# Performance work log

Hardware: AMD Instinct MI355X
Metric: run time of the kernel (lower is better)

The kernel has to match this reference:

```python
import jax, jax.numpy as jnp
import numpy as np

B, S, H = 4, 1024, 2048
NQ, NKV, D = 32, 4, 128
EPS = 1e-6
THETA = 1e6


def setup_inputs() -> dict:
    key = jax.random.key(0)
    k1, k2, k3 = jax.random.split(key, 3)
    hidden = jax.random.normal(k1, (B, S, H), jnp.float32) * 0.02
    w_qkv = jax.random.normal(k2, (H, (NQ + 2 * NKV) * D), jnp.float32) * 0.02
    w_o = jax.random.normal(k3, (NQ * D, H), jnp.float32) * 0.02
    q_norm_w = jnp.ones((D,), jnp.float32)
    k_norm_w = jnp.ones((D,), jnp.float32)
    # rotary tables, broadcast to [B, S, D]
    inv_freq = 1.0 / (THETA ** (jnp.arange(0, D, 2, dtype=jnp.float32) / D))
    freqs = jnp.arange(S, dtype=jnp.float32)[:, None] * inv_freq[None, :]  # [S, D/2]
    emb = jnp.concatenate([freqs, freqs], axis=-1)  # [S, D]
    cos = jnp.broadcast_to(jnp.cos(emb)[None], (B, S, D))
    sin = jnp.broadcast_to(jnp.sin(emb)[None], (B, S, D))
    return {"hidden": hidden, "w_qkv": w_qkv, "w_o": w_o,
            "q_norm_w": q_norm_w, "k_norm_w": k_norm_w, "cos": cos, "sin": sin}


def _rms_norm(x, w):
    xf = x.astype(jnp.float32)
    var = jnp.mean(xf * xf, axis=-1, keepdims=True)
    return (w * (xf * jax.lax.rsqrt(var + EPS))).astype(x.dtype)


def _rotate_half(x):
    h = x.shape[-1] // 2
    return jnp.concatenate([-x[..., h:], x[..., :h]], axis=-1)


def reference(hidden, w_qkv, w_o, q_norm_w, k_norm_w, cos, sin):
    b, s, _ = hidden.shape
    qkv = jnp.einsum('bsh,he->bse', hidden, w_qkv)
    q = qkv[..., : NQ * D].reshape(b, s, NQ, D)
    k = qkv[..., NQ * D: (NQ + NKV) * D].reshape(b, s, NKV, D)
    v = qkv[..., (NQ + NKV) * D:].reshape(b, s, NKV, D)

    # per-head RMSNorm on Q and K
    q = _rms_norm(q, q_norm_w)
    k = _rms_norm(k, k_norm_w)

    # fused RoPE (rotate-half), cos/sin broadcast over heads
    c = cos[:, :, None, :]
    sn = sin[:, :, None, :]
    q = q * c + _rotate_half(q) * sn
    k = k * c + _rotate_half(k) * sn

    # GQA causal flash-attention (prefill, sparse_mode=3 -> causal)
    g = NQ // NKV
    qg = q.reshape(b, s, NKV, g, D)
    scale = 1.0 / jnp.sqrt(jnp.asarray(D, hidden.dtype))
    scores = jnp.einsum('bqkgd,bskd->bkgqs', qg, k) * scale  # [B,NKV,g,S,S]
    causal = jnp.tril(jnp.ones((s, s), bool))
    scores = jnp.where(causal[None, None, None], scores, jnp.finfo(scores.dtype).min)
    probs = jax.nn.softmax(scores, axis=-1)
    out = jnp.einsum('bkgqs,bskd->bqkgd', probs, v).reshape(b, s, NQ * D)
    return jnp.einsum('bse,eh->bsh', out, w_o)
```

## Files before the change

kernel.cpp:

```cpp
#include <hip/hip_runtime.h>

#define BB 4
#define SS 1024
#define HH 2048
#define NQH 32
#define NKVH 4
#define DD 128
#define EQKV 5120

typedef __attribute__((ext_vector_type(8))) short s8v;
typedef __attribute__((ext_vector_type(4))) short s4v;
typedef __attribute__((ext_vector_type(4))) float f4v;

__device__ __forceinline__ unsigned short f2bf(float f) {
  unsigned int u = __builtin_bit_cast(unsigned int, f);
  u += 0x7fffu + ((u >> 16) & 1u);
  return (unsigned short)(u >> 16);
}
__device__ __forceinline__ float bf2f(unsigned short s) {
  unsigned int u = ((unsigned int)s) << 16;
  return __builtin_bit_cast(float, u);
}

__device__ __forceinline__ void async16(unsigned short* lds, const unsigned short* g) {
  __builtin_amdgcn_global_load_lds(
      (const __attribute__((address_space(1))) unsigned int*)g,
      (__attribute__((address_space(3))) unsigned int*)lds, 16, 0, 0);
}


__global__ __launch_bounds__(256) void cvt_bf16(const float* __restrict__ in,
                                                unsigned short* __restrict__ out, int n) {
  int i = (blockIdx.x * 256 + threadIdx.x) * 4;
  if (i >= n) return;
  f4v v = *reinterpret_cast<const f4v*>(in + i);
  s4v o;
#pragma unroll
  for (int j = 0; j < 4; ++j) o[j] = (short)f2bf(v[j]);
  *reinterpret_cast<s4v*>(out + i) = o;
}

__global__ __launch_bounds__(256) void transpose_cvt(const float* __restrict__ in,
                                                     unsigned short* __restrict__ out,
                                                     int K, int N) {
  __shared__ unsigned short T[64][65];
  const int k0 = blockIdx.y * 64, n0 = blockIdx.x * 64;
  const int t = threadIdx.x;
  const int r = t >> 4, c4 = (t & 15) * 4;
#pragma unroll
  for (int i = 0; i < 4; ++i) {
    f4v v = *reinterpret_cast<const f4v*>(&in[(size_t)(k0 + r + i * 16) * N + n0 + c4]);
#pragma unroll
    for (int j = 0; j < 4; ++j) T[r + i * 16][c4 + j] = f2bf(v[j]);
  }
  __syncthreads();
#pragma unroll
  for (int i = 0; i < 4; ++i) {
    int n = r + i * 16;
    s4v o;
#pragma unroll
    for (int j = 0; j < 4; ++j) o[j] = (short)T[c4 + j][n];
    *reinterpret_cast<s4v*>(&out[(size_t)(n0 + n) * K + k0 + c4]) = o;
  }
}

__global__ __launch_bounds__(256) void vtrans(const unsigned short* __restrict__ qkv,
                                              unsigned short* __restrict__ Vt) {
  __shared__ unsigned short T[64][68];
  const int s0 = blockIdx.x * 64;
  const int d0 = blockIdx.y * 64;
  const int bk = blockIdx.z;
  const int b = bk >> 2, hkv = bk & 3;
  const int t = threadIdx.x;
  const int r = t >> 4, c4 = (t & 15) * 4;
  const unsigned short* src = qkv + (size_t)(b * SS + s0) * EQKV + (NQH + NKVH + hkv) * DD + d0;
#pragma unroll
  for (int i = 0; i < 4; ++i) {
    int s = r + i * 16;
    s4v v = *reinterpret_cast<const s4v*>(src + (size_t)s * EQKV + c4);
    *reinterpret_cast<s4v*>(&T[s][c4]) = v;
  }
  __syncthreads();
#pragma unroll
  for (int i = 0; i < 4; ++i) {
    int d = r + i * 16;
    s4v o;
#pragma unroll
    for (int j = 0; j < 4; ++j) o[j] = (short)T[c4 + j][d];
    *reinterpret_cast<s4v*>(&Vt[((size_t)bk * DD + d0 + d) * SS + s0 + c4]) = o;
  }
}

template <bool CF32>
__global__ __launch_bounds__(256) void gemm_128(const unsigned short* __restrict__ A,
                                                const unsigned short* __restrict__ Bt,
                                                void* __restrict__ Cp,
                                                int M, int N, int K, int lda) {
  __shared__ unsigned short BUF[2][16384];
  const int tid = threadIdx.x;
  const int ln = tid & 63, w = tid >> 6;
  const int la = ln & 15, quad = ln >> 4;
  const int wm = (w >> 1) * 64, wn = (w & 1) * 64;

  const int G = gridDim.x, cpx = G >> 3;
  const int swz = (blockIdx.x & 7) * cpx + (blockIdx.x >> 3);
  const int ytiles = M >> 7;
  const int by = swz % ytiles, bx = swz / ytiles;
  const int m0 = by * 128, n0 = bx * 128;

  f4v acc[4][4] = {};

  const int srow = w * 32 + (ln >> 3);
  const int sch = ((ln & 7) ^ ((ln >> 3) & 7)) * 8;
  const unsigned short* pA = A + (size_t)(m0 + srow) * lda + sch;
  const unsigned short* pB = Bt + (size_t)(n0 + srow) * K + sch;

#define STAGE(bf, koff)                                                        \
  _Pragma("unroll") for (int j = 0; j < 4; ++j) {                              \
    async16(&BUF[bf][(w * 4 + j) * 512], pA + (size_t)(j * 8) * lda + (koff)); \
    async16(&BUF[bf][8192 + (w * 4 + j) * 512], pB + (size_t)(j * 8) * K + (koff)); \
  }

  STAGE(0, 0)
  __syncthreads();

  const int NT = K >> 6;
  int cur = 0;
  for (int t = 0; t < NT; ++t) {
    const int kn = (t + 1 < NT) ? (t + 1) * 64 : t * 64;
    STAGE(cur ^ 1, kn)
    s8v a[4][2], b[4][2];
#pragma unroll
    for (int f = 0; f < 4; ++f)
#pragma unroll
      for (int kh = 0; kh < 2; ++kh) {
        const int slot = ((kh * 4 + quad) ^ (la & 7)) * 8;
        a[f][kh] = *reinterpret_cast<const s8v*>(&BUF[cur][(wm + f * 16 + la) * 64 + slot]);
        b[f][kh] = *reinterpret_cast<const s8v*>(&BUF[cur][8192 + (wn + f * 16 + la) * 64 + slot]);
      }
    __builtin_amdgcn_s_setprio(1);
#pragma unroll
    for (int kh = 0; kh < 2; ++kh)
#pragma unroll
      for (int mf = 0; mf < 4; ++mf)
#pragma unroll
        for (int nf = 0; nf < 4; ++nf)
          acc[mf][nf] = __builtin_amdgcn_mfma_f32_16x16x32_bf16(a[mf][kh], b[nf][kh], acc[mf][nf], 0, 0, 0);
    __builtin_amdgcn_s_setprio(0);
    __syncthreads();
    cur ^= 1;
  }
#undef STAGE

#pragma unroll
  for (int mf = 0; mf < 4; ++mf)
#pragma unroll
    for (int nf = 0; nf < 4; ++nf)
#pragma unroll
      for (int r = 0; r < 4; ++r) {
        int row = m0 + wm + mf * 16 + quad * 4 + r;
        int col = n0 + wn + nf * 16 + la;
        if constexpr (CF32) ((float*)Cp)[(size_t)row * N + col] = acc[mf][nf][r];
        else ((unsigned short*)Cp)[(size_t)row * N + col] = f2bf(acc[mf][nf][r]);
      }
}

__global__ __launch_bounds__(512) void attn2(unsigned short* __restrict__ qkv,
                                             const unsigned short* __restrict__ Vt) {
  const int idx = blockIdx.x;
  const int tile = 7 - (idx >> 7);
  const int h = idx & 31;
  const int b = (idx >> 5) & 3;
  const int hkv = h >> 3;
  const int tid = threadIdx.x;
  const int ln = tid & 63, w = tid >> 6;
  const int la = ln & 15, quad = ln >> 4;
  const int qr0 = tile * 128;
  __shared__ unsigned short Ks[64 * 128];
  __shared__ unsigned short Vts[128 * 64];
  __shared__ unsigned short Ps[8][16][64];

  const size_t rowb = (size_t)b * SS;
  const int wq0 = qr0 + w * 16;
  const int wqb = wq0 & ~63;
  s8v qf[4];
  {
    const unsigned short* qrow = qkv + (rowb + wq0 + la) * EQKV + h * DD;
#pragma unroll
    for (int t = 0; t < 4; ++t) qf[t] = *reinterpret_cast<const s8v*>(qrow + t * 32 + quad * 8);
  }
  const unsigned short* kcol = qkv + (NQH + hkv) * DD;
  const unsigned short* vtb = Vt + (size_t)(b * NKVH + hkv) * DD * SS;

  float m_[4], ls[4];
  f4v acc[8] = {};
#pragma unroll
  for (int r = 0; r < 4; ++r) { m_[r] = -1.0e30f; ls[r] = 0.f; }

  const float SC = 0.08838834764831845f;
  const int nkb = 2 * tile + 2;
  for (int kb = 0; kb < nkb; ++kb) {
    const int key0 = kb * 64;
    __syncthreads();
#pragma unroll
    for (int i = 0; i < 2; ++i) {
      int row = w * 8 + i * 4 + (ln >> 4);
      int chunk = (ln & 15) ^ (row & 15);
      async16(&Ks[(w * 8 + i * 4) * 128],
              kcol + (rowb + key0 + row) * EQKV + chunk * 8);
    }
#pragma unroll
    for (int i = 0; i < 2; ++i) {
      int row = w * 16 + i * 8 + (ln >> 3);
      int chunk = (ln & 7) ^ (ln >> 3);
      async16(&Vts[(w * 16 + i * 8) * 64],
              vtb + (size_t)row * SS + key0 + chunk * 8);
    }
    __syncthreads();
    if (key0 > wqb) continue;
    f4v sc[4];
#pragma unroll
    for (int kt = 0; kt < 4; ++kt) {
      f4v z = {};
#pragma unroll
      for (int t = 0; t < 4; ++t) {
        s8v kf = *reinterpret_cast<const s8v*>(&Ks[(kt * 16 + la) * 128 + ((t * 4 + quad) ^ la) * 8]);
        z = __builtin_amdgcn_mfma_f32_16x16x32_bf16(qf[t], kf, z, 0, 0, 0);
      }
      sc[kt] = z;
    }
    const bool diag = (key0 == wqb);
    float pmax[4];
#pragma unroll
    for (int r = 0; r < 4; ++r) {
      if (diag) {
        int q = wq0 + quad * 4 + r;
#pragma unroll
        for (int kt = 0; kt < 4; ++kt)
          if (key0 + kt * 16 + la > q) sc[kt][r] = -1.0e30f;
      }
      pmax[r] = fmaxf(fmaxf(sc[0][r], sc[1][r]), fmaxf(sc[2][r], sc[3][r]));
    }
    int need = 0;
#pragma unroll
    for (int r = 0; r < 4; ++r) need |= (pmax[r] > m_[r] + 64.0f) ? 1 : 0;
    if (__any(need)) {
#pragma unroll
      for (int r = 0; r < 4; ++r) {
        float mx = pmax[r];
#pragma unroll
        for (int off = 8; off >= 1; off >>= 1) mx = fmaxf(mx, __shfl_xor(mx, off));
        float mnew = fmaxf(m_[r], mx);
        float al = __expf((m_[r] - mnew) * SC);
        m_[r] = mnew;
        ls[r] *= al;
#pragma unroll
        for (int nt = 0; nt < 8; ++nt) acc[nt][r] *= al;
      }
    }
#pragma unroll
    for (int r = 0; r < 4; ++r) {
      const int row = quad * 4 + r;
      const float mS = m_[r] * SC;
#pragma unroll
      for (int kt = 0; kt < 4; ++kt) {
        float p = __expf(__builtin_fmaf(sc[kt][r], SC, -mS));
        ls[r] += p;
        int col = kt * 16 + la;
        Ps[w][row][(((col >> 3) ^ (row & 7)) << 3) | (col & 7)] = f2bf(p);
      }
    }
#pragma unroll
    for (int c = 0; c < 2; ++c) {
      s8v pf = *reinterpret_cast<const s8v*>(&Ps[w][la][(((c * 4 + quad) ^ (la & 7)) << 3)]);
#pragma unroll
      for (int nt = 0; nt < 8; ++nt) {
        s8v vf = *reinterpret_cast<const s8v*>(
            &Vts[(nt * 16 + la) * 64 + ((c * 4 + quad) ^ (la & 7)) * 8]);
        acc[nt] = __builtin_amdgcn_mfma_f32_16x16x32_bf16(pf, vf, acc[nt], 0, 0, 0);
      }
    }
  }
#pragma unroll
  for (int r = 0; r < 4; ++r)
#pragma unroll
    for (int off = 8; off >= 1; off >>= 1) ls[r] += __shfl_xor(ls[r], off);
#pragma unroll
  for (int nt = 0; nt < 8; ++nt)
#pragma unroll
    for (int r = 0; r < 4; ++r) {
      int q = wq0 + quad * 4 + r;
      qkv[(rowb + q) * EQKV + h * DD + nt * 16 + la] = f2bf(acc[nt][r] / ls[r]);
    }
}

template <bool AF32, bool BF32, bool CF32>
__global__ __launch_bounds__(256) void gemm_t(const void* __restrict__ Ap,
                                              const void* __restrict__ Bp,
                                              void* __restrict__ Cp,
                                              int M, int N, int K, int lda) {
  __shared__ unsigned short As[64][40];
  __shared__ unsigned short Bs[64][40];
  const int tid  = threadIdx.x;
  const int lane = tid & 63;
  const int wave = tid >> 6;
  const int la   = lane & 15;
  const int quad = lane >> 4;
  const int m0 = blockIdx.y * 64;
  const int n0 = blockIdx.x * 64;
  const int wm = (wave >> 1) * 32;
  const int wn = (wave & 1) * 32;
  f4v acc[2][2] = {};
  const int ar = tid >> 2, ac = (tid & 3) * 8;
  const int bk = tid >> 3, bn = (tid & 7) * 8;
  for (int k0 = 0; k0 < K; k0 += 32) {
    s8v av;
    if constexpr (AF32) {
      const float* a = (const float*)Ap + (size_t)(m0 + ar) * lda + ac + k0;
      f4v v0 = *reinterpret_cast<const f4v*>(a);
      f4v v1 = *reinterpret_cast<const f4v*>(a + 4);
#pragma unroll
      for (int j = 0; j < 4; ++j) { av[j] = (short)f2bf(v0[j]); av[j + 4] = (short)f2bf(v1[j]); }
    } else {
      av = *reinterpret_cast<const s8v*>((const unsigned short*)Ap + (size_t)(m0 + ar) * lda + ac + k0);
    }
    unsigned short bvs[8];
    if constexpr (BF32) {
      const float* bp = (const float*)Bp + (size_t)(k0 + bk) * N + n0 + bn;
      f4v v0 = *reinterpret_cast<const f4v*>(bp);
      f4v v1 = *reinterpret_cast<const f4v*>(bp + 4);
#pragma unroll
      for (int j = 0; j < 4; ++j) { bvs[j] = f2bf(v0[j]); bvs[j + 4] = f2bf(v1[j]); }
    } else {
      s8v bv = *reinterpret_cast<const s8v*>((const unsigned short*)Bp + (size_t)(k0 + bk) * N + n0 + bn);
#pragma unroll
      for (int j = 0; j < 8; ++j) bvs[j] = (unsigned short)bv[j];
    }
    *reinterpret_cast<s8v*>(&As[ar][ac]) = av;
#pragma unroll
    for (int j = 0; j < 8; ++j) Bs[bn + j][bk] = bvs[j];
    __syncthreads();
#pragma unroll
    for (int mi = 0; mi < 2; ++mi) {
      s8v af = *reinterpret_cast<const s8v*>(&As[wm + mi * 16 + la][quad * 8]);
#pragma unroll
      for (int ni = 0; ni < 2; ++ni) {
        s8v bfr = *reinterpret_cast<const s8v*>(&Bs[wn + ni * 16 + la][quad * 8]);
        acc[mi][ni] = __builtin_amdgcn_mfma_f32_16x16x32_bf16(af, bfr, acc[mi][ni], 0, 0, 0);
      }
    }
    __syncthreads();
  }
#pragma unroll
  for (int mi = 0; mi < 2; ++mi)
#pragma unroll
    for (int ni = 0; ni < 2; ++ni)
#pragma unroll
      for (int r = 0; r < 4; ++r) {
        int row = m0 + wm + mi * 16 + quad * 4 + r;
        int col = n0 + wn + ni * 16 + la;
        if constexpr (CF32) ((float*)Cp)[(size_t)row * N + col] = acc[mi][ni][r];
        else ((unsigned short*)Cp)[(size_t)row * N + col] = f2bf(acc[mi][ni][r]);
      }
}

__global__ __launch_bounds__(64) void attn_slow(unsigned short* __restrict__ qkv) {
  const int tile = blockIdx.x;
  const int h = blockIdx.y;
  const int b = blockIdx.z;
  const int hkv = h >> 3;
  const int lane = threadIdx.x;
  const int la = lane & 15;
  const int quad = lane >> 4;
  const int qr0 = tile * 16;
  __shared__ unsigned short P[16][32];
  __shared__ unsigned short V[32][128];
  const size_t base = (size_t)b * SS * EQKV;
  s8v qf[4];
  {
    const unsigned short* qrow = qkv + base + (size_t)(qr0 + la) * EQKV + h * DD;
#pragma unroll
    for (int t = 0; t < 4; ++t)
      qf[t] = *reinterpret_cast<const s8v*>(qrow + t * 32 + quad * 8);
  }
  const unsigned short* kbase = qkv + base + (NQH + hkv) * DD;
  const unsigned short* vbase = qkv + base + (NQH + NKVH + hkv) * DD;
  float m[4], l[4], al[4];
  f4v acc[8] = {};
#pragma unroll
  for (int r = 0; r < 4; ++r) { m[r] = -1.0e30f; l[r] = 0.f; }
  const float scale = 0.08838834764831845f;
  const int nkb = (qr0 + 16 + 31) >> 5;
  for (int kb = 0; kb < nkb; ++kb) {
    const int key0 = kb * 32;
    __syncthreads();
#pragma unroll
    for (int i = 0; i < 8; ++i) {
      int c = i * 64 + lane;
      int row = c >> 4, col = (c & 15) * 8;
      *reinterpret_cast<s8v*>(&V[row][col]) =
          *reinterpret_cast<const s8v*>(vbase + (size_t)(key0 + row) * EQKV + col);
    }
    f4v s0 = {}, s1 = {};
#pragma unroll
    for (int t = 0; t < 4; ++t) {
      s8v k0f = *reinterpret_cast<const s8v*>(kbase + (size_t)(key0 + la) * EQKV + t * 32 + quad * 8);
      s8v k1f = *reinterpret_cast<const s8v*>(kbase + (size_t)(key0 + 16 + la) * EQKV + t * 32 + quad * 8);
      s0 = __builtin_amdgcn_mfma_f32_16x16x32_bf16(qf[t], k0f, s0, 0, 0, 0);
      s1 = __builtin_amdgcn_mfma_f32_16x16x32_bf16(qf[t], k1f, s1, 0, 0, 0);
    }
#pragma unroll
    for (int r = 0; r < 4; ++r) {
      int q = qr0 + quad * 4 + r;
      float v0 = (key0 + la <= q) ? s0[r] * scale : -1.0e30f;
      float v1 = (key0 + 16 + la <= q) ? s1[r] * scale : -1.0e30f;
      float mx = fmaxf(v0, v1);
#pragma unroll
      for (int off = 8; off >= 1; off >>= 1) mx = fmaxf(mx, __shfl_xor(mx, off));
      float mnew = fmaxf(m[r], mx);
      float p0 = __expf(v0 - mnew);
      float p1 = __expf(v1 - mnew);
      al[r] = __expf(m[r] - mnew);
      m[r] = mnew;
      float rsum = p0 + p1;
#pragma unroll
      for (int off = 8; off >= 1; off >>= 1) rsum += __shfl_xor(rsum, off);
      l[r] = l[r] * al[r] + rsum;
      P[quad * 4 + r][la] = f2bf(p0);
      P[quad * 4 + r][la + 16] = f2bf(p1);
    }
#pragma unroll
    for (int nt = 0; nt < 8; ++nt)
#pragma unroll
      for (int r = 0; r < 4; ++r) acc[nt][r] *= al[r];
    __syncthreads();
    s8v pf = *reinterpret_cast<const s8v*>(&P[la][quad * 8]);
#pragma unroll
    for (int nt = 0; nt < 8; ++nt) {
      s8v vf;
#pragma unroll
      for (int j = 0; j < 8; ++j)
        vf[j] = (short)V[quad * 8 + j][nt * 16 + la];
      acc[nt] = __builtin_amdgcn_mfma_f32_16x16x32_bf16(pf, vf, acc[nt], 0, 0, 0);
    }
  }
#pragma unroll
  for (int nt = 0; nt < 8; ++nt)
#pragma unroll
    for (int r = 0; r < 4; ++r) {
      int q = qr0 + quad * 4 + r;
      qkv[base + (size_t)q * EQKV + h * DD + nt * 16 + la] = f2bf(acc[nt][r] / l[r]);
    }
}

__global__ __launch_bounds__(256) void norm_rope(unsigned short* __restrict__ qkv,
                                                 const float* __restrict__ qw,
                                                 const float* __restrict__ kw,
                                                 const float* __restrict__ cosp,
                                                 const float* __restrict__ sinp) {
  const int h = blockIdx.x;
  const int bs = blockIdx.y * 4 + (threadIdx.x >> 6);
  const int s = bs & (SS - 1);
  const int lane = threadIdx.x & 63;
  const int d0 = lane * 2;
  unsigned short* p = qkv + (size_t)bs * EQKV + h * DD + d0;
  unsigned int u = *reinterpret_cast<const unsigned int*>(p);
  float x0 = bf2f((unsigned short)(u & 0xffff));
  float x1 = bf2f((unsigned short)(u >> 16));
  float ss = x0 * x0 + x1 * x1;
#pragma unroll
  for (int off = 32; off >= 1; off >>= 1) ss += __shfl_xor(ss, off);
  float rs = rsqrtf(ss * (1.0f / 128.0f) + 1e-6f);
  const float* w = (h < NQH) ? qw : kw;
  float n0 = x0 * rs * w[d0];
  float n1 = x1 * rs * w[d0 + 1];
  float o0 = __shfl_xor(n0, 32);
  float o1 = __shfl_xor(n1, 32);
  float r0 = (lane < 32) ? -o0 : o0;
  float r1 = (lane < 32) ? -o1 : o1;
  float c0 = cosp[(size_t)s * DD + d0], c1 = cosp[(size_t)s * DD + d0 + 1];
  float s0 = sinp[(size_t)s * DD + d0], s1 = sinp[(size_t)s * DD + d0 + 1];
  float y0 = n0 * c0 + r0 * s0;
  float y1 = n1 * c1 + r1 * s1;
  unsigned int outv = (unsigned int)f2bf(y0) | ((unsigned int)f2bf(y1) << 16);
  *reinterpret_cast<unsigned int*>(p) = outv;
}

extern "C" void kernel_launch(void* const* d_in, const int* in_sizes, int n_in,
                              void* d_out, int out_size, void* d_ws, size_t ws_size,
                              hipStream_t stream) {
  const float* hidden = (const float*)d_in[0];
  const float* w_qkv  = (const float*)d_in[1];
  const float* w_o    = (const float*)d_in[2];
  const float* q_w    = (const float*)d_in[3];
  const float* k_w    = (const float*)d_in[4];
  const float* cosp   = (const float*)d_in[5];
  const float* sinp   = (const float*)d_in[6];
  float* out = (float*)d_out;

  const int M = BB * SS;
  const size_t szHid  = (size_t)M * HH;
  const size_t szWqkv = (size_t)HH * EQKV;
  const size_t szWo   = (size_t)(NQH * DD) * HH;
  const size_t szQkv  = (size_t)M * EQKV;
  const size_t need = (szHid + szWqkv + szWo + szQkv) * sizeof(unsigned short);

  if (ws_size >= need) {
    unsigned short* hb16  = (unsigned short*)d_ws;
    unsigned short* wqkvT = hb16 + szHid;
    unsigned short* woT   = wqkvT + szWqkv;
    unsigned short* qkv   = woT + szWo;
    unsigned short* Vt    = hb16;

    cvt_bf16<<<(int)(szHid / 1024), 256, 0, stream>>>(hidden, hb16, (int)szHid);
    transpose_cvt<<<dim3(EQKV / 64, HH / 64), 256, 0, stream>>>(w_qkv, wqkvT, HH, EQKV);
    transpose_cvt<<<dim3(HH / 64, (NQH * DD) / 64), 256, 0, stream>>>(w_o, woT, NQH * DD, HH);

    gemm_128<false><<<(M / 128) * (EQKV / 128), 256, 0, stream>>>(
        hb16, wqkvT, qkv, M, EQKV, HH, HH);
    vtrans<<<dim3(SS / 64, DD / 64, BB * NKVH), 256, 0, stream>>>(qkv, Vt);
    norm_rope<<<dim3(NQH + NKVH, M / 4), 256, 0, stream>>>(qkv, q_w, k_w, cosp, sinp);
    attn2<<<1024, 512, 0, stream>>>(qkv, Vt);
    gemm_128<true><<<(M / 128) * (HH / 128), 256, 0, stream>>>(
        qkv, woT, out, M, HH, NQH * DD, EQKV);
  } else {
    unsigned short* qkvb = (unsigned short*)d_ws;
    for (int b = 0; b < BB; ++b) {
      const float* hb = hidden + (size_t)b * SS * HH;
      float* ob = out + (size_t)b * SS * HH;
      gemm_t<true, true, false><<<dim3(EQKV / 64, SS / 64), 256, 0, stream>>>(
          hb, w_qkv, qkvb, SS, EQKV, HH, HH);
      norm_rope<<<dim3(NQH + NKVH, SS / 4), 256, 0, stream>>>(qkvb, q_w, k_w, cosp, sinp);
      attn_slow<<<dim3(SS / 16, NQH, 1), 64, 0, stream>>>(qkvb);
      gemm_t<false, true, true><<<dim3(HH / 64, SS / 64), 256, 0, stream>>>(
          qkvb, w_o, ob, SS, HH, NQH * DD, EQKV);
    }
  }
}
```

Baseline: 424.4 us.

## Fuse hidden fp32-to-bf16 conversion into QKV GEMM and Q norm/RoPE into attention

Removes the separate hidden-state bf16 conversion kernel. The QKV GEMM now loads fp32 A tiles into registers, converts them to bf16 and writes them to LDS after the MFMA block, overlapping the global loads with compute. Q-head RMSNorm and RoPE move into the attention kernel's Q fragment load, so norm_rope only processes the 4 K heads. This saves one full pass over hidden and the Q region of qkv. The cost is twice the A-operand global traffic inside the GEMM, more register pressure, and a synchronous load path in place of async LDS copies for A.

```diff
diff --git a/kernel.cpp b/kernel.cpp
--- a/kernel.cpp
+++ b/kernel.cpp
@@ -28,17 +28,6 @@
       (__attribute__((address_space(3))) unsigned int*)lds, 16, 0, 0);
 }
 
-
-__global__ __launch_bounds__(256) void cvt_bf16(const float* __restrict__ in,
-                                                unsigned short* __restrict__ out, int n) {
-  int i = (blockIdx.x * 256 + threadIdx.x) * 4;
-  if (i >= n) return;
-  f4v v = *reinterpret_cast<const f4v*>(in + i);
-  s4v o;
-#pragma unroll
-  for (int j = 0; j < 4; ++j) o[j] = (short)f2bf(v[j]);
-  *reinterpret_cast<s4v*>(out + i) = o;
-}
 
 __global__ __launch_bounds__(256) void transpose_cvt(const float* __restrict__ in,
                                                      unsigned short* __restrict__ out,
@@ -91,8 +80,8 @@
   }
 }
 
-template <bool CF32>
-__global__ __launch_bounds__(256) void gemm_128(const unsigned short* __restrict__ A,
+template <bool AF32, bool CF32>
+__global__ __launch_bounds__(256) void gemm_128(const void* __restrict__ Ap,
                                                 const unsigned short* __restrict__ Bt,
                                                 void* __restrict__ Cp,
                                                 int M, int N, int K, int lda) {
@@ -112,23 +101,58 @@
 
   const int srow = w * 32 + (ln >> 3);
   const int sch = ((ln & 7) ^ ((ln >> 3) & 7)) * 8;
-  const unsigned short* pA = A + (size_t)(m0 + srow) * lda + sch;
+  const unsigned short* pAh =
+      AF32 ? nullptr : (const unsigned short*)Ap + (size_t)(m0 + srow) * lda + sch;
+  const float* pAf =
+      AF32 ? (const float*)Ap + (size_t)(m0 + srow) * lda + (ln & 7) * 8 : nullptr;
   const unsigned short* pB = Bt + (size_t)(n0 + srow) * K + sch;
-
-#define STAGE(bf, koff)                                                        \
-  _Pragma("unroll") for (int j = 0; j < 4; ++j) {                              \
-    async16(&BUF[bf][(w * 4 + j) * 512], pA + (size_t)(j * 8) * lda + (koff)); \
-    async16(&BUF[bf][8192 + (w * 4 + j) * 512], pB + (size_t)(j * 8) * K + (koff)); \
-  }
-
-  STAGE(0, 0)
+  const int awr = srow * 64 + sch;
+
+#define STAGE_B(bf, koff)                                                           \
+  _Pragma("unroll") for (int j = 0; j < 4; ++j)                                     \
+    async16(&BUF[bf][8192 + (w * 4 + j) * 512], pB + (size_t)(j * 8) * K + (koff));
+#define STAGE_AH(bf, koff)                                                          \
+  _Pragma("unroll") for (int j = 0; j < 4; ++j)                                     \
+    async16(&BUF[bf][(w * 4 + j) * 512], pAh + (size_t)(j * 8) * lda + (koff));
+#define LOAD_AF(koff)                                                               \
+  _Pragma("unroll") for (int j = 0; j < 4; ++j) {                                   \
+    const float* p = pAf + (size_t)(j * 8) * lda + (koff);                          \
+    va[j][0] = *reinterpret_cast<const f4v*>(p);                                    \
+    va[j][1] = *reinterpret_cast<const f4v*>(p + 4);                                \
+  }
+#define WRITE_AF(bf)                                                                \
+  _Pragma("unroll") for (int j = 0; j < 4; ++j) {                                   \
+    s8v o;                                                                          \
+    _Pragma("unroll") for (int c = 0; c < 4; ++c) o[c] = (short)f2bf(va[j][0][c]);  \
+    _Pragma("unroll") for (int c = 0; c < 4; ++c) o[c + 4] = (short)f2bf(va[j][1][c]); \
+    *reinterpret_cast<s8v*>(&BUF[bf][awr + j * 512]) = o;                           \
+  }
+
+  {
+    f4v va[4][2];
+    if constexpr (AF32) {
+      LOAD_AF(0)
+      STAGE_B(0, 0)
+      WRITE_AF(0)
+    } else {
+      STAGE_AH(0, 0)
+      STAGE_B(0, 0)
+    }
+  }
   __syncthreads();
 
   const int NT = K >> 6;
   int cur = 0;
   for (int t = 0; t < NT; ++t) {
     const int kn = (t + 1 < NT) ? (t + 1) * 64 : t * 64;
-    STAGE(cur ^ 1, kn)
+    f4v va[4][2];
+    if constexpr (AF32) {
+      LOAD_AF(kn)
+      STAGE_B(cur ^ 1, kn)
+    } else {
+      STAGE_AH(cur ^ 1, kn)
+      STAGE_B(cur ^ 1, kn)
+    }
     s8v a[4][2], b[4][2];
 #pragma unroll
     for (int f = 0; f < 4; ++f)
@@ -147,10 +171,14 @@
         for (int nf = 0; nf < 4; ++nf)
           acc[mf][nf] = __builtin_amdgcn_mfma_f32_16x16x32_bf16(a[mf][kh], b[nf][kh], acc[mf][nf], 0, 0, 0);
     __builtin_amdgcn_s_setprio(0);
+    if constexpr (AF32) { WRITE_AF(cur ^ 1) }
     __syncthreads();
     cur ^= 1;
   }
-#undef STAGE
+#undef STAGE_B
+#undef STAGE_AH
+#undef LOAD_AF
+#undef WRITE_AF
 
 #pragma unroll
   for (int mf = 0; mf < 4; ++mf)
@@ -166,7 +194,10 @@
 }
 
 __global__ __launch_bounds__(512) void attn2(unsigned short* __restrict__ qkv,
-                                             const unsigned short* __restrict__ Vt) {
+                                             const unsigned short* __restrict__ Vt,
+                                             const float* __restrict__ qnw,
+                                             const float* __restrict__ cosp,
+                                             const float* __restrict__ sinp) {
   const int idx = blockIdx.x;
   const int tile = 7 - (idx >> 7);
   const int h = idx & 31;
@@ -186,8 +217,46 @@
   s8v qf[4];
   {
     const unsigned short* qrow = qkv + (rowb + wq0 + la) * EQKV + h * DD;
-#pragma unroll
-    for (int t = 0; t < 4; ++t) qf[t] = *reinterpret_cast<const s8v*>(qrow + t * 32 + quad * 8);
+    float xf[4][8];
+    float ss = 0.f;
+#pragma unroll
+    for (int t = 0; t < 4; ++t) {
+      s8v v = *reinterpret_cast<const s8v*>(qrow + t * 32 + quad * 8);
+#pragma unroll
+      for (int j = 0; j < 8; ++j) {
+        xf[t][j] = bf2f((unsigned short)v[j]);
+        ss += xf[t][j] * xf[t][j];
+      }
+    }
+    ss += __shfl_xor(ss, 16);
+    ss += __shfl_xor(ss, 32);
+    const float rs = rsqrtf(ss * (1.0f / 128.0f) + 1e-6f);
+    float n[4][8];
+#pragma unroll
+    for (int t = 0; t < 4; ++t) {
+      const int d0 = t * 32 + quad * 8;
+      f4v w0 = *reinterpret_cast<const f4v*>(qnw + d0);
+      f4v w1 = *reinterpret_cast<const f4v*>(qnw + d0 + 4);
+#pragma unroll
+      for (int j = 0; j < 8; ++j)
+        n[t][j] = xf[t][j] * rs * (j < 4 ? w0[j] : w1[j - 4]);
+    }
+    const int s = wq0 + la;
+#pragma unroll
+    for (int t = 0; t < 4; ++t) {
+      const int d0 = t * 32 + quad * 8;
+      f4v c0 = *reinterpret_cast<const f4v*>(cosp + (size_t)s * DD + d0);
+      f4v c1 = *reinterpret_cast<const f4v*>(cosp + (size_t)s * DD + d0 + 4);
+      f4v sn0 = *reinterpret_cast<const f4v*>(sinp + (size_t)s * DD + d0);
+      f4v sn1 = *reinterpret_cast<const f4v*>(sinp + (size_t)s * DD + d0 + 4);
+#pragma unroll
+      for (int j = 0; j < 8; ++j) {
+        float rot = (t < 2) ? -n[t + 2][j] : n[t - 2][j];
+        float cc = (j < 4) ? c0[j] : c1[j - 4];
+        float sv = (j < 4) ? sn0[j] : sn1[j - 4];
+        qf[t][j] = (short)f2bf(n[t][j] * cc + rot * sv);
+      }
+    }
   }
   const unsigned short* kcol = qkv + (NQH + hkv) * DD;
   const unsigned short* vtb = Vt + (size_t)(b * NKVH + hkv) * DD * SS;
@@ -457,8 +526,9 @@
                                                  const float* __restrict__ qw,
                                                  const float* __restrict__ kw,
                                                  const float* __restrict__ cosp,
-                                                 const float* __restrict__ sinp) {
-  const int h = blockIdx.x;
+                                                 const float* __restrict__ sinp,
+                                                 int h0) {
+  const int h = h0 + blockIdx.x;
   const int bs = blockIdx.y * 4 + (threadIdx.x >> 6);
   const int s = bs & (SS - 1);
   const int lane = threadIdx.x & 63;
@@ -512,16 +582,15 @@
     unsigned short* qkv   = woT + szWo;
     unsigned short* Vt    = hb16;
 
-    cvt_bf16<<<(int)(szHid / 1024), 256, 0, stream>>>(hidden, hb16, (int)szHid);
     transpose_cvt<<<dim3(EQKV / 64, HH / 64), 256, 0, stream>>>(w_qkv, wqkvT, HH, EQKV);
     transpose_cvt<<<dim3(HH / 64, (NQH * DD) / 64), 256, 0, stream>>>(w_o, woT, NQH * DD, HH);
 
-    gemm_128<false><<<(M / 128) * (EQKV / 128), 256, 0, stream>>>(
-        hb16, wqkvT, qkv, M, EQKV, HH, HH);
+    gemm_128<true, false><<<(M / 128) * (EQKV / 128), 256, 0, stream>>>(
+        hidden, wqkvT, qkv, M, EQKV, HH, HH);
     vtrans<<<dim3(SS / 64, DD / 64, BB * NKVH), 256, 0, stream>>>(qkv, Vt);
-    norm_rope<<<dim3(NQH + NKVH, M / 4), 256, 0, stream>>>(qkv, q_w, k_w, cosp, sinp);
-    attn2<<<1024, 512, 0, stream>>>(qkv, Vt);
-    gemm_128<true><<<(M / 128) * (HH / 128), 256, 0, stream>>>(
+    norm_rope<<<dim3(NKVH, M / 4), 256, 0, stream>>>(qkv, q_w, k_w, cosp, sinp, NQH);
+    attn2<<<1024, 512, 0, stream>>>(qkv, Vt, q_w, cosp, sinp);
+    gemm_128<false, true><<<(M / 128) * (HH / 128), 256, 0, stream>>>(
         qkv, woT, out, M, HH, NQH * DD, EQKV);
   } else {
     unsigned short* qkvb = (unsigned short*)d_ws;
@@ -530,7 +599,7 @@
       float* ob = out + (size_t)b * SS * HH;
       gemm_t<true, true, false><<<dim3(EQKV / 64, SS / 64), 256, 0, stream>>>(
           hb, w_qkv, qkvb, SS, EQKV, HH, HH);
-      norm_rope<<<dim3(NQH + NKVH, SS / 4), 256, 0, stream>>>(qkvb, q_w, k_w, cosp, sinp);
+      norm_rope<<<dim3(NQH + NKVH, SS / 4), 256, 0, stream>>>(qkvb, q_w, k_w, cosp, sinp, 0);
       attn_slow<<<dim3(SS / 16, NQH, 1), 64, 0, stream>>>(qkvb);
       gemm_t<false, true, true><<<dim3(HH / 64, SS / 64), 256, 0, stream>>>(
           qkvb, w_o, ob, SS, HH, NQH * DD, EQKV);
```

Measured after the change: 493.6 us. 1.16x slower.
